# Kernel tuning notes

Measured on AMD Instinct MI355X. Metric: run time of the kernel, lower is better.

The kernel has to match this reference:

```python
import jax, jax.numpy as jnp
import numpy as np

N_TOKENS = 32768
DIM = 4096
N_EXPERTS = 64
TOPK = 2
UPDATE_BIAS_RATE = 0.001
ROUTE_SCALE = 1.0


def setup_inputs() -> dict:
    key = jax.random.key(0)
    k1, k2 = jax.random.split(key)
    x = jax.random.normal(k1, (N_TOKENS, DIM), dtype=jnp.float32)
    # gate projection weight, as in nn.Parameter(torch.empty(E, dim)) + kaiming init
    weight = jax.random.normal(k2, (N_EXPERTS, DIM), dtype=jnp.float32) * 0.02
    bias = jnp.zeros((N_EXPERTS,), dtype=jnp.float32)          # registered buffer
    target_dist = jnp.full((N_EXPERTS,), 1.0 / N_EXPERTS, dtype=jnp.float32)
    return {"x": x, "weight": weight, "bias": bias, "target_dist": target_dist}


def reference(x, weight, bias, target_dist):
    # scores = linear(nan_to_num(x), W) + bias, softmax in fp32
    xc = jnp.nan_to_num(x, nan=0.0)
    scores = (xc @ weight.T + bias).astype(jnp.float32)        # [N, E]
    probs = jax.nn.softmax(scores, axis=-1)                    # [N, E]
    # top-k: gathered values equal the top-k probabilities
    topv, indices = jax.lax.top_k(probs, TOPK)                 # [N, K], [N, K]
    weights = topv / jnp.sum(topv, axis=-1, keepdims=True)
    weights = weights * ROUTE_SCALE
    # load-balancing stats: bincount with float weights == segment_sum
    expert_weights_sum = jax.ops.segment_sum(
        weights.reshape(-1), indices.reshape(-1), num_segments=N_EXPERTS)
    total_weights = expert_weights_sum.sum()
    load_error = target_dist * total_weights - expert_weights_sum
    new_bias = bias + UPDATE_BIAS_RATE * (load_error / total_weights)
    return weights.astype(x.dtype), indices, new_bias
```

## Files before the change

### kernel.cpp

```cpp
#include <hip/hip_runtime.h>
#include <math.h>

#define N_TOKENS 32768
#define DIM      4096
#define NE       64
#define TM       64
#define BK       128
#define KHALF    (DIM / 2)
#define NBLK_MAIN (N_TOKENS / TM * 2)
#define NBLK_POST (N_TOKENS / 256)
#define EPS_GAP  2e-3f
#define REFINE_BLOCKS 1024

#define WOFF     65664
#define WL_OFF   16384
#define PART_OFF 128
#define PSC_OFF  524288
#define WFRAG_ELEMS (512 * 512)

typedef __bf16 bf16x8 __attribute__((ext_vector_type(8)));
typedef float  f32x16 __attribute__((ext_vector_type(16)));

__global__ __launch_bounds__(256) void prep_w(
    const float* __restrict__ w, float* __restrict__ ws)
{
    __bf16* whi = (__bf16*)(ws + WOFF);
    __bf16* wlo = whi + WFRAG_ELEMS;
    const int tid  = blockIdx.x * 256 + threadIdx.x;
    const int f    = tid >> 6, lane = tid & 63;
    const int nt   = f & 1,    K16  = f >> 1;
    const int e    = nt * 32 + (lane & 31);
    const int k    = K16 * 16 + (lane >> 5) * 8;
    const float4 a = *(const float4*)(w + (size_t)e * DIM + k);
    const float4 b = *(const float4*)(w + (size_t)e * DIM + k + 4);
    const float v[8] = {a.x, a.y, a.z, a.w, b.x, b.y, b.z, b.w};
    __bf16 h[8], l[8];
    #pragma unroll
    for (int i = 0; i < 8; ++i) {
        h[i] = (__bf16)v[i];
        l[i] = (__bf16)(v[i] - (float)h[i]);
    }
    *(bf16x8*)(whi + (size_t)tid * 8) = *(bf16x8*)h;
    *(bf16x8*)(wlo + (size_t)tid * 8) = *(bf16x8*)l;
}

__device__ __forceinline__ unsigned pack_pair(float f0, float f1, float& r0, float& r1) {
    const unsigned u0 = __float_as_uint(f0), u1 = __float_as_uint(f1);
    const unsigned h0 = u0 & 0xFFFF0000u,   h1 = u1 & 0xFFFF0000u;
    r0 = f0 - __uint_as_float(h0);
    r1 = f1 - __uint_as_float(h1);
    return (u0 >> 16) | h1;
}
__device__ __forceinline__ void cvt8(const float4 a, const float4 b, uint4& h, uint4& l) {
    float r0, r1, r2, r3, r4, r5, r6, r7;
    h.x = pack_pair(a.x, a.y, r0, r1);
    h.y = pack_pair(a.z, a.w, r2, r3);
    h.z = pack_pair(b.x, b.y, r4, r5);
    h.w = pack_pair(b.z, b.w, r6, r7);
    l.x = (__float_as_uint(r0) >> 16) | (__float_as_uint(r1) & 0xFFFF0000u);
    l.y = (__float_as_uint(r2) >> 16) | (__float_as_uint(r3) & 0xFFFF0000u);
    l.z = (__float_as_uint(r4) >> 16) | (__float_as_uint(r5) & 0xFFFF0000u);
    l.w = (__float_as_uint(r6) >> 16) | (__float_as_uint(r7) & 0xFFFF0000u);
}

__device__ __forceinline__ void gload_lds16(const float* g, float* lds) {
    __builtin_amdgcn_global_load_lds(
        (const __attribute__((address_space(1))) unsigned*)g,
        (__attribute__((address_space(3))) unsigned*)lds, 16, 0, 0);
}

__global__ __launch_bounds__(256) void gate_main(
    const float* __restrict__ x, float* __restrict__ ws)
{
    __shared__ __align__(16) float xs[TM * BK];

    const __bf16* whi = (const __bf16*)(ws + WOFF);
    const __bf16* wlo = whi + WFRAG_ELEMS;
    float*        psc = ws + PSC_OFF;

    const int t    = threadIdx.x;
    const int lane = t & 63;
    const int wave = t >> 6;
    const int mt   = wave >> 1;
    const int nt   = wave & 1;
    const int kh   = blockIdx.x & 1;
    const int tb   = (blockIdx.x >> 1) * TM;
    const int kbeg = kh * KHALF;

    const int l31 = lane & 31, lhi = lane >> 5;

    size_t sbase[8];
    #pragma unroll
    for (int wl = 0; wl < 8; ++wl) {
        const int row = wave * 16 + wl * 2 + lhi;
        const int col = l31 ^ (row & 31);
        sbase[wl] = (size_t)(tb + row) * DIM + kbeg + col * 4;
    }

    const int a_row = mt * 32 + l31;

    f32x16 acc0, acc12;
    #pragma unroll
    for (int i = 0; i < 16; ++i) { acc0[i] = 0.f; acc12[i] = 0.f; }

    for (int s = 0; s < KHALF / BK; ++s) {
        #pragma unroll
        for (int wl = 0; wl < 8; ++wl)
            gload_lds16(x + sbase[wl] + s * BK, &xs[(wave * 16 + wl * 2) * BK]);
        __syncthreads();

        const int K16c = (kbeg + s * BK) >> 4;
        #pragma unroll
        for (int ks = 0; ks < 8; ++ks) {
            const int s0 = ks * 4 + (lhi << 1);
            const float4 fa = *(const float4*)&xs[a_row * BK + ((s0 ^ l31) << 2)];
            const float4 fb = *(const float4*)&xs[a_row * BK + (((s0 + 1) ^ l31) << 2)];
            uint4 h, l;
            cvt8(fa, fb, h, l);
            const size_t bidx = ((size_t)((K16c + ks) * 2 + nt) * 64 + lane) * 8;
            const bf16x8 bh = *(const bf16x8*)(whi + bidx);
            const bf16x8 bl = *(const bf16x8*)(wlo + bidx);
            const bf16x8 ah = __builtin_bit_cast(bf16x8, h);
            const bf16x8 al = __builtin_bit_cast(bf16x8, l);
            acc0  = __builtin_amdgcn_mfma_f32_32x32x16_bf16(ah, bh, acc0,  0, 0, 0);
            acc12 = __builtin_amdgcn_mfma_f32_32x32x16_bf16(al, bh, acc12, 0, 0, 0);
            acc12 = __builtin_amdgcn_mfma_f32_32x32x16_bf16(ah, bl, acc12, 0, 0, 0);
        }
        __syncthreads();
    }

    float* p = psc + (size_t)kh * N_TOKENS * NE + (size_t)tb * NE;
    #pragma unroll
    for (int r = 0; r < 16; ++r) {
        const int tok = mt * 32 + (r & 3) + 8 * (r >> 2) + 4 * lhi;
        p[(size_t)tok * NE + nt * 32 + l31] = acc0[r] + acc12[r];
    }
}

__global__ __launch_bounds__(256) void gate_post(
    const float* __restrict__ bias,
    float* __restrict__ out,
    float* __restrict__ ws)
{
    __shared__ float sbias[NE];
    __shared__ float part[NE];
    unsigned* wl_count = (unsigned*)(ws + 64);
    float*    partials = ws + PART_OFF;
    int*      wl       = (int*)(ws + WL_OFF);
    const float* psc   = ws + PSC_OFF;
    const size_t PL    = (size_t)N_TOKENS * NE;

    const int t = threadIdx.x;
    if (t < NE) { sbias[t] = bias[t]; part[t] = 0.f; }
    __syncthreads();

    const int tok = blockIdx.x * 256 + t;
    const float* p = psc + (size_t)tok * NE;

    float v1 = -3e38f, v2 = -3e38f, v3 = -3e38f;
    int   i1 = 0,      i2 = 0;
    #pragma unroll
    for (int g = 0; g < 16; ++g) {
        const float4 a = *(const float4*)(p + g * 4);
        const float4 b = *(const float4*)(p + PL + g * 4);
        float sv4[4] = {a.x + b.x, a.y + b.y, a.z + b.z, a.w + b.w};
        #pragma unroll
        for (int j = 0; j < 4; ++j) {
            const float sv = sv4[j] + sbias[g * 4 + j];
            const int   e  = g * 4 + j;
            if (sv > v1)      { v3 = v2; v2 = v1; i2 = i1; v1 = sv; i1 = e; }
            else if (sv > v2) { v3 = v2; v2 = sv; i2 = e; }
            else if (sv > v3) { v3 = sv; }
        }
    }
    const bool risky = (v1 - v2 < EPS_GAP) || (v2 - v3 < EPS_GAP);
    if (risky) {
        const int pos = (int)atomicAdd(wl_count, 1u);
        wl[pos] = tok;
    } else {
        const float ex = expf(v2 - v1);
        const float w1 = 1.f / (1.f + ex);
        const float w2 = ex * w1;
        const size_t g = (size_t)tok * 2;
        *(float2*)(out + g)                        = make_float2(w1, w2);
        *(float2*)(out + (size_t)N_TOKENS * 2 + g) = make_float2((float)i1, (float)i2);
        atomicAdd(&part[i1], w1);
        atomicAdd(&part[i2], w2);
    }
    __syncthreads();
    if (t < NE) partials[(size_t)blockIdx.x * NE + t] = part[t];
}

__global__ __launch_bounds__(256) void gate_refine(
    const float* __restrict__ x,
    const float* __restrict__ w,
    const float* __restrict__ bias,
    float* __restrict__ out,
    float* __restrict__ ws)
{
    float*          ews_ref  = ws;
    const unsigned* wl_count = (const unsigned*)(ws + 64);
    const int*      wl       = (const int*)(ws + WL_OFF);

    const int t = threadIdx.x;
    const int e = t >> 2;
    const int q = t & 3;
    __shared__ double sc[NE];

    const unsigned count = *wl_count;
    for (unsigned it = blockIdx.x; it < count; it += gridDim.x) {
        const int tok = wl[it];
        const float* xr = x + (size_t)tok * DIM;
        const float* wr = w + (size_t)e * DIM;
        double s = 0.0;
        const int k0 = q * (DIM / 4), k1 = k0 + DIM / 4;
        for (int k = k0; k < k1; k += 4) {
            const float4 a = *(const float4*)(xr + k);
            const float4 b = *(const float4*)(wr + k);
            s += (double)a.x * (double)b.x;
            s += (double)a.y * (double)b.y;
            s += (double)a.z * (double)b.z;
            s += (double)a.w * (double)b.w;
        }
        s += __shfl_xor(s, 1);
        s += __shfl_xor(s, 2);
        if (q == 0) sc[e] = s + (double)bias[e];
        __syncthreads();

        if (t == 0) {
            double v1 = -1e300, v2 = -1e300;
            int i1 = 0, i2 = 0;
            for (int j = 0; j < NE; ++j) {
                const double sv = sc[j];
                if (sv > v1)      { v2 = v1; i2 = i1; v1 = sv; i1 = j; }
                else if (sv > v2) { v2 = sv; i2 = j; }
            }
            const double ex = exp(v2 - v1);
            const double w1 = 1.0 / (1.0 + ex);
            const double w2 = ex * w1;
            const size_t g = (size_t)tok * 2;
            *(float2*)(out + g)                        = make_float2((float)w1, (float)w2);
            *(float2*)(out + (size_t)N_TOKENS * 2 + g) = make_float2((float)i1, (float)i2);
            atomicAdd(&ews_ref[i1], (float)w1);
            atomicAdd(&ews_ref[i2], (float)w2);
        }
        __syncthreads();
    }
}

__global__ void gate_bias(
    const float* __restrict__ bias,
    const float* __restrict__ target,
    const float* __restrict__ ws,
    float* __restrict__ out)
{
    const int e = threadIdx.x;
    const float* partials = ws + PART_OFF;
    float v = ws[e];
    for (int b = 0; b < NBLK_POST; ++b) v += partials[(size_t)b * NE + e];
    float total = v;
    #pragma unroll
    for (int off = 32; off > 0; off >>= 1)
        total += __shfl_xor(total, off);
    const float nb = bias[e] + 0.001f * ((target[e] * total - v) / total);
    out[(size_t)N_TOKENS * 4 + e] = nb;
}

extern "C" void kernel_launch(void* const* d_in, const int* in_sizes, int n_in,
                              void* d_out, int out_size, void* d_ws, size_t ws_size,
                              hipStream_t stream) {
    const float* x      = (const float*)d_in[0];
    const float* w      = (const float*)d_in[1];
    const float* bias   = (const float*)d_in[2];
    const float* target = (const float*)d_in[3];
    float* out = (float*)d_out;
    float* ws  = (float*)d_ws;

    hipMemsetAsync(ws, 0, 128 * sizeof(float), stream);
    prep_w     <<<128, 256, 0, stream>>>(w, ws);
    gate_main  <<<NBLK_MAIN, 256, 0, stream>>>(x, ws);
    gate_post  <<<NBLK_POST, 256, 0, stream>>>(bias, out, ws);
    gate_refine<<<REFINE_BLOCKS, 256, 0, stream>>>(x, w, bias, out, ws);
    gate_bias  <<<1, 64, 0, stream>>>(bias, target, ws, out);
}
```

Measured before the change: 298.1 us.

## Fuse top-k epilogue into GEMM kernel, drop split-K, double-buffer LDS loads

Removes the split-K partial-score buffer and the separate gate_post kernel. Each block now computes the full K reduction for 64 tokens and runs the top-2 selection and routing weights from scores held in shared memory. The x tiles are streamed with a two-stage LDS double buffer using async global-to-LDS loads, explicit vmcnt waits and barriers, so loads overlap the MFMA work. This cuts global traffic for the scores and one launch, at the cost of half as many blocks and a serialized 64-thread top-k epilogue per block.

Measured after the change: 302.5 us. About the same (+1.5%).

```diff
diff --git a/kernel.cpp b/kernel.cpp
--- a/kernel.cpp
+++ b/kernel.cpp
@@ -5,21 +5,22 @@
 #define DIM      4096
 #define NE       64
 #define TM       64
-#define BK       128
-#define KHALF    (DIM / 2)
-#define NBLK_MAIN (N_TOKENS / TM * 2)
-#define NBLK_POST (N_TOKENS / 256)
+#define BK       64
+#define CHUNKS   (DIM / BK)
+#define NBLK     (N_TOKENS / TM)
 #define EPS_GAP  2e-3f
 #define REFINE_BLOCKS 1024
 
 #define WOFF     65664
-#define WL_OFF   16384
+#define WL_OFF   32896
 #define PART_OFF 128
-#define PSC_OFF  524288
 #define WFRAG_ELEMS (512 * 512)
 
 typedef __bf16 bf16x8 __attribute__((ext_vector_type(8)));
 typedef float  f32x16 __attribute__((ext_vector_type(16)));
+
+#define SCHED0() __builtin_amdgcn_sched_barrier(0)
+#define BAR()    __builtin_amdgcn_s_barrier()
 
 __global__ __launch_bounds__(256) void prep_w(
     const float* __restrict__ w, float* __restrict__ ws)
@@ -70,51 +71,64 @@
 }
 
 __global__ __launch_bounds__(256) void gate_main(
-    const float* __restrict__ x, float* __restrict__ ws)
-{
-    __shared__ __align__(16) float xs[TM * BK];
-
-    const __bf16* whi = (const __bf16*)(ws + WOFF);
-    const __bf16* wlo = whi + WFRAG_ELEMS;
-    float*        psc = ws + PSC_OFF;
+    const float* __restrict__ x, const float* __restrict__ bias,
+    float* __restrict__ out, float* __restrict__ ws)
+{
+    __shared__ __align__(16) float xs[2][TM * BK];
+    __shared__ float sc[TM][68];
+    __shared__ float part[NE];
+    __shared__ float sbias[NE];
+
+    const __bf16* whi  = (const __bf16*)(ws + WOFF);
+    const __bf16* wlo  = whi + WFRAG_ELEMS;
+    unsigned* wl_count = (unsigned*)(ws + 64);
+    float*    partials = ws + PART_OFF;
+    int*      wl       = (int*)(ws + WL_OFF);
 
     const int t    = threadIdx.x;
     const int lane = t & 63;
     const int wave = t >> 6;
     const int mt   = wave >> 1;
     const int nt   = wave & 1;
-    const int kh   = blockIdx.x & 1;
-    const int tb   = (blockIdx.x >> 1) * TM;
-    const int kbeg = kh * KHALF;
-
-    const int l31 = lane & 31, lhi = lane >> 5;
-
-    size_t sbase[8];
-    #pragma unroll
-    for (int wl = 0; wl < 8; ++wl) {
-        const int row = wave * 16 + wl * 2 + lhi;
-        const int col = l31 ^ (row & 31);
-        sbase[wl] = (size_t)(tb + row) * DIM + kbeg + col * 4;
+    const int tb   = blockIdx.x * TM;
+    const int l31  = lane & 31, lhi = lane >> 5;
+
+    if (t < NE) { sbias[t] = bias[t]; part[t] = 0.f; }
+
+    size_t sofs[4];
+    int    dofs[4];
+    #pragma unroll
+    for (int gl = 0; gl < 4; ++gl) {
+        const int row  = wave * 16 + gl * 4 + (lane >> 4);
+        const int slot = (lane & 15) ^ (row & 15);
+        sofs[gl] = (size_t)(tb + row) * DIM + slot * 4;
+        dofs[gl] = (wave * 16 + gl * 4) * BK;
     }
 
     const int a_row = mt * 32 + l31;
+    const int abase = a_row * BK;
+    const int aswz  = a_row & 15;
 
     f32x16 acc0, acc12;
     #pragma unroll
     for (int i = 0; i < 16; ++i) { acc0[i] = 0.f; acc12[i] = 0.f; }
 
-    for (int s = 0; s < KHALF / BK; ++s) {
+    #pragma unroll
+    for (int gl = 0; gl < 4; ++gl) gload_lds16(x + sofs[gl],      &xs[0][dofs[gl]]);
+    #pragma unroll
+    for (int gl = 0; gl < 4; ++gl) gload_lds16(x + sofs[gl] + BK, &xs[1][dofs[gl]]);
+
+    for (int c = 0; c < CHUNKS; ++c) {
+        if (c < CHUNKS - 1) { asm volatile("s_waitcnt vmcnt(4)" ::: "memory"); }
+        else                { asm volatile("s_waitcnt vmcnt(0)" ::: "memory"); }
+        SCHED0(); BAR(); SCHED0();
+
+        const int K16c = c * 4;
         #pragma unroll
-        for (int wl = 0; wl < 8; ++wl)
-            gload_lds16(x + sbase[wl] + s * BK, &xs[(wave * 16 + wl * 2) * BK]);
-        __syncthreads();
-
-        const int K16c = (kbeg + s * BK) >> 4;
-        #pragma unroll
-        for (int ks = 0; ks < 8; ++ks) {
-            const int s0 = ks * 4 + (lhi << 1);
-            const float4 fa = *(const float4*)&xs[a_row * BK + ((s0 ^ l31) << 2)];
-            const float4 fb = *(const float4*)&xs[a_row * BK + (((s0 + 1) ^ l31) << 2)];
+        for (int ks = 0; ks < 4; ++ks) {
+            const int s0 = ks * 4 + lhi * 2;
+            const float4 fa = *(const float4*)&xs[c & 1][abase + ((s0 ^ aswz) << 2)];
+            const float4 fb = *(const float4*)&xs[c & 1][abase + (((s0 + 1) ^ aswz) << 2)];
             uint4 h, l;
             cvt8(fa, fb, h, l);
             const size_t bidx = ((size_t)((K16c + ks) * 2 + nt) * 64 + lane) * 8;
@@ -126,66 +140,49 @@
             acc12 = __builtin_amdgcn_mfma_f32_32x32x16_bf16(al, bh, acc12, 0, 0, 0);
             acc12 = __builtin_amdgcn_mfma_f32_32x32x16_bf16(ah, bl, acc12, 0, 0, 0);
         }
-        __syncthreads();
-    }
-
-    float* p = psc + (size_t)kh * N_TOKENS * NE + (size_t)tb * NE;
+
+        SCHED0(); BAR(); SCHED0();
+        if (c < CHUNKS - 2) {
+            const size_t cofs = (size_t)(c + 2) * BK;
+            #pragma unroll
+            for (int gl = 0; gl < 4; ++gl)
+                gload_lds16(x + sofs[gl] + cofs, &xs[c & 1][dofs[gl]]);
+        }
+    }
+
+    const int e = nt * 32 + l31;
     #pragma unroll
     for (int r = 0; r < 16; ++r) {
         const int tok = mt * 32 + (r & 3) + 8 * (r >> 2) + 4 * lhi;
-        p[(size_t)tok * NE + nt * 32 + l31] = acc0[r] + acc12[r];
-    }
-}
-
-__global__ __launch_bounds__(256) void gate_post(
-    const float* __restrict__ bias,
-    float* __restrict__ out,
-    float* __restrict__ ws)
-{
-    __shared__ float sbias[NE];
-    __shared__ float part[NE];
-    unsigned* wl_count = (unsigned*)(ws + 64);
-    float*    partials = ws + PART_OFF;
-    int*      wl       = (int*)(ws + WL_OFF);
-    const float* psc   = ws + PSC_OFF;
-    const size_t PL    = (size_t)N_TOKENS * NE;
-
-    const int t = threadIdx.x;
-    if (t < NE) { sbias[t] = bias[t]; part[t] = 0.f; }
+        sc[tok][e] = acc0[r] + acc12[r];
+    }
     __syncthreads();
 
-    const int tok = blockIdx.x * 256 + t;
-    const float* p = psc + (size_t)tok * NE;
-
-    float v1 = -3e38f, v2 = -3e38f, v3 = -3e38f;
-    int   i1 = 0,      i2 = 0;
-    #pragma unroll
-    for (int g = 0; g < 16; ++g) {
-        const float4 a = *(const float4*)(p + g * 4);
-        const float4 b = *(const float4*)(p + PL + g * 4);
-        float sv4[4] = {a.x + b.x, a.y + b.y, a.z + b.z, a.w + b.w};
-        #pragma unroll
-        for (int j = 0; j < 4; ++j) {
-            const float sv = sv4[j] + sbias[g * 4 + j];
-            const int   e  = g * 4 + j;
-            if (sv > v1)      { v3 = v2; v2 = v1; i2 = i1; v1 = sv; i1 = e; }
-            else if (sv > v2) { v3 = v2; v2 = sv; i2 = e; }
-            else if (sv > v3) { v3 = sv; }
-        }
-    }
-    const bool risky = (v1 - v2 < EPS_GAP) || (v2 - v3 < EPS_GAP);
-    if (risky) {
-        const int pos = (int)atomicAdd(wl_count, 1u);
-        wl[pos] = tok;
-    } else {
-        const float ex = expf(v2 - v1);
-        const float w1 = 1.f / (1.f + ex);
-        const float w2 = ex * w1;
-        const size_t g = (size_t)tok * 2;
-        *(float2*)(out + g)                        = make_float2(w1, w2);
-        *(float2*)(out + (size_t)N_TOKENS * 2 + g) = make_float2((float)i1, (float)i2);
-        atomicAdd(&part[i1], w1);
-        atomicAdd(&part[i2], w2);
+    if (t < TM) {
+        const int tok = t;
+        float v1 = -3e38f, v2 = -3e38f, v3 = -3e38f;
+        int   i1 = 0,      i2 = 0;
+        #pragma unroll 8
+        for (int ei = 0; ei < NE; ++ei) {
+            const float s = sc[tok][ei] + sbias[ei];
+            if (s > v1)      { v3 = v2; v2 = v1; i2 = i1; v1 = s; i1 = ei; }
+            else if (s > v2) { v3 = v2; v2 = s;  i2 = ei; }
+            else if (s > v3) { v3 = s; }
+        }
+        const bool risky = (v1 - v2 < EPS_GAP) || (v2 - v3 < EPS_GAP);
+        if (risky) {
+            const int pos = (int)atomicAdd(wl_count, 1u);
+            wl[pos] = tb + tok;
+        } else {
+            const float ex = expf(v2 - v1);
+            const float w1 = 1.f / (1.f + ex);
+            const float w2 = ex * w1;
+            const size_t g = (size_t)(tb + tok) * 2;
+            *(float2*)(out + g)                        = make_float2(w1, w2);
+            *(float2*)(out + (size_t)N_TOKENS * 2 + g) = make_float2((float)i1, (float)i2);
+            atomicAdd(&part[i1], w1);
+            atomicAdd(&part[i2], w2);
+        }
     }
     __syncthreads();
     if (t < NE) partials[(size_t)blockIdx.x * NE + t] = part[t];
@@ -257,7 +254,7 @@
     const int e = threadIdx.x;
     const float* partials = ws + PART_OFF;
     float v = ws[e];
-    for (int b = 0; b < NBLK_POST; ++b) v += partials[(size_t)b * NE + e];
+    for (int b = 0; b < NBLK; ++b) v += partials[(size_t)b * NE + e];
     float total = v;
     #pragma unroll
     for (int off = 32; off > 0; off >>= 1)
@@ -278,8 +275,7 @@
 
     hipMemsetAsync(ws, 0, 128 * sizeof(float), stream);
     prep_w     <<<128, 256, 0, stream>>>(w, ws);
-    gate_main  <<<NBLK_MAIN, 256, 0, stream>>>(x, ws);
-    gate_post  <<<NBLK_POST, 256, 0, stream>>>(bias, out, ws);
+    gate_main  <<<NBLK, 256, 0, stream>>>(x, bias, out, ws);
     gate_refine<<<REFINE_BLOCKS, 256, 0, stream>>>(x, w, bias, out, ws);
     gate_bias  <<<1, 64, 0, stream>>>(bias, target, ws, out);
 }
```

## Restructure gate GEMM into 4-way K split with double-buffered async staging

Applied to the files above, without the earlier changes.

Rewrites the main gate GEMM kernel to split K four ways across blocks, with 128-thread blocks where each wave owns 32 tokens and all 64 experts. X tiles are double-buffered through LDS with direct global-to-LDS loads, and W fragments are prefetched into registers, using explicit waitcnt and scheduling barriers so loads overlap MFMA work. The aim is to hide memory latency on the bandwidth-bound x read without block-wide syncs. In exchange, the score partials workspace grows from two to four planes, so the post kernel must read twice as much partial data.

Measured after the change: 296.0 us. Within noise of the previous version (-0.7%).

```diff
diff --git a/kernel.cpp b/kernel.cpp
--- a/kernel.cpp
+++ b/kernel.cpp
@@ -4,10 +4,11 @@
 #define N_TOKENS 32768
 #define DIM      4096
 #define NE       64
-#define TM       64
-#define BK       128
-#define KHALF    (DIM / 2)
-#define NBLK_MAIN (N_TOKENS / TM * 2)
+#define KS       4
+#define KSPAN    (DIM / KS)
+#define BKF      32
+#define NCH      (KSPAN / BKF)
+#define NBLK_MAIN (N_TOKENS / 64 * KS)
 #define NBLK_POST (N_TOKENS / 256)
 #define EPS_GAP  2e-3f
 #define REFINE_BLOCKS 1024
@@ -20,6 +21,8 @@
 
 typedef __bf16 bf16x8 __attribute__((ext_vector_type(8)));
 typedef float  f32x16 __attribute__((ext_vector_type(16)));
+
+#define SB0() __builtin_amdgcn_sched_barrier(0)
 
 __global__ __launch_bounds__(256) void prep_w(
     const float* __restrict__ w, float* __restrict__ ws)
@@ -69,10 +72,12 @@
         (__attribute__((address_space(3))) unsigned*)lds, 16, 0, 0);
 }
 
-__global__ __launch_bounds__(256) void gate_main(
+struct BS { bf16x8 h[2][2]; bf16x8 l[2][2]; };
+
+__global__ __launch_bounds__(128) void gate_main(
     const float* __restrict__ x, float* __restrict__ ws)
 {
-    __shared__ __align__(16) float xs[TM * BK];
+    __shared__ __align__(16) float xsf[4096];
 
     const __bf16* whi = (const __bf16*)(ws + WOFF);
     const __bf16* wlo = whi + WFRAG_ELEMS;
@@ -80,60 +85,96 @@
 
     const int t    = threadIdx.x;
     const int lane = t & 63;
-    const int wave = t >> 6;
-    const int mt   = wave >> 1;
-    const int nt   = wave & 1;
-    const int kh   = blockIdx.x & 1;
-    const int tb   = (blockIdx.x >> 1) * TM;
-    const int kbeg = kh * KHALF;
-
-    const int l31 = lane & 31, lhi = lane >> 5;
-
-    size_t sbase[8];
-    #pragma unroll
-    for (int wl = 0; wl < 8; ++wl) {
-        const int row = wave * 16 + wl * 2 + lhi;
-        const int col = l31 ^ (row & 31);
-        sbase[wl] = (size_t)(tb + row) * DIM + kbeg + col * 4;
-    }
-
-    const int a_row = mt * 32 + l31;
-
-    f32x16 acc0, acc12;
-    #pragma unroll
-    for (int i = 0; i < 16; ++i) { acc0[i] = 0.f; acc12[i] = 0.f; }
-
-    for (int s = 0; s < KHALF / BK; ++s) {
-        #pragma unroll
-        for (int wl = 0; wl < 8; ++wl)
-            gload_lds16(x + sbase[wl] + s * BK, &xs[(wave * 16 + wl * 2) * BK]);
-        __syncthreads();
-
-        const int K16c = (kbeg + s * BK) >> 4;
-        #pragma unroll
-        for (int ks = 0; ks < 8; ++ks) {
-            const int s0 = ks * 4 + (lhi << 1);
-            const float4 fa = *(const float4*)&xs[a_row * BK + ((s0 ^ l31) << 2)];
-            const float4 fb = *(const float4*)&xs[a_row * BK + (((s0 + 1) ^ l31) << 2)];
-            uint4 h, l;
-            cvt8(fa, fb, h, l);
-            const size_t bidx = ((size_t)((K16c + ks) * 2 + nt) * 64 + lane) * 8;
-            const bf16x8 bh = *(const bf16x8*)(whi + bidx);
-            const bf16x8 bl = *(const bf16x8*)(wlo + bidx);
-            const bf16x8 ah = __builtin_bit_cast(bf16x8, h);
-            const bf16x8 al = __builtin_bit_cast(bf16x8, l);
-            acc0  = __builtin_amdgcn_mfma_f32_32x32x16_bf16(ah, bh, acc0,  0, 0, 0);
-            acc12 = __builtin_amdgcn_mfma_f32_32x32x16_bf16(al, bh, acc12, 0, 0, 0);
-            acc12 = __builtin_amdgcn_mfma_f32_32x32x16_bf16(ah, bl, acc12, 0, 0, 0);
-        }
-        __syncthreads();
-    }
-
-    float* p = psc + (size_t)kh * N_TOKENS * NE + (size_t)tb * NE;
+    const int w    = t >> 6;
+    const int tile = blockIdx.x >> 2;
+    const int kq   = blockIdx.x & 3;
+    const int tb   = tile * 64 + w * 32;
+    const int kbeg = kq * KSPAN;
+    const int l31  = lane & 31, lhi = lane >> 5;
+    const int dbase = w * 2048;
+
+    size_t sofs[4];
+    #pragma unroll
+    for (int g = 0; g < 4; ++g) {
+        const int row = g * 8 + (lane >> 3);
+        const int col = ((lane & 7) ^ (lane >> 3)) * 4;
+        sofs[g] = (size_t)(tb + row) * DIM + kbeg + col;
+    }
+
+    const int arow  = l31;
+    const int aswz  = arow & 7;
+
+    f32x16 acc0, acc1;
+    #pragma unroll
+    for (int i = 0; i < 16; ++i) { acc0[i] = 0.f; acc1[i] = 0.f; }
+
+    BS BA, BB;
+
+    #define LOADB(B, c) {                                                     \
+        _Pragma("unroll")                                                     \
+        for (int ks = 0; ks < 2; ++ks) {                                      \
+            _Pragma("unroll")                                                 \
+            for (int nt = 0; nt < 2; ++nt) {                                  \
+                const size_t f = (size_t)((kq * 64 + (c) * 2 + ks) * 2 + nt); \
+                (B).h[ks][nt] = *(const bf16x8*)(whi + (f * 64 + lane) * 8);  \
+                (B).l[ks][nt] = *(const bf16x8*)(wlo + (f * 64 + lane) * 8);  \
+            }                                                                 \
+        } }
+
+    #define STAGE(c, p) {                                                     \
+        _Pragma("unroll")                                                     \
+        for (int g = 0; g < 4; ++g)                                           \
+            gload_lds16(x + sofs[g] + (size_t)(c) * BKF,                      \
+                        &xsf[dbase + (p) * 1024 + g * 256]); }
+
+    #define COMPUTE(p, B) {                                                   \
+        const int ab = dbase + (p) * 1024 + arow * 32;                        \
+        _Pragma("unroll")                                                     \
+        for (int ks = 0; ks < 2; ++ks) {                                      \
+            const int s0 = ks * 4 + lhi * 2;                                  \
+            const float4 fa = *(const float4*)&xsf[ab + ((s0 ^ aswz) << 2)];  \
+            const float4 fb = *(const float4*)&xsf[ab + (((s0+1) ^ aswz) << 2)]; \
+            uint4 hh, ll;                                                     \
+            cvt8(fa, fb, hh, ll);                                             \
+            const bf16x8 ah = __builtin_bit_cast(bf16x8, hh);                 \
+            const bf16x8 al = __builtin_bit_cast(bf16x8, ll);                 \
+            acc0 = __builtin_amdgcn_mfma_f32_32x32x16_bf16(ah, (B).h[ks][0], acc0, 0,0,0); \
+            acc1 = __builtin_amdgcn_mfma_f32_32x32x16_bf16(ah, (B).h[ks][1], acc1, 0,0,0); \
+            acc0 = __builtin_amdgcn_mfma_f32_32x32x16_bf16(al, (B).h[ks][0], acc0, 0,0,0); \
+            acc1 = __builtin_amdgcn_mfma_f32_32x32x16_bf16(al, (B).h[ks][1], acc1, 0,0,0); \
+            acc0 = __builtin_amdgcn_mfma_f32_32x32x16_bf16(ah, (B).l[ks][0], acc0, 0,0,0); \
+            acc1 = __builtin_amdgcn_mfma_f32_32x32x16_bf16(ah, (B).l[ks][1], acc1, 0,0,0); \
+        } }
+
+    LOADB(BA, 0); STAGE(0, 0); LOADB(BB, 1); STAGE(1, 1);
+
+    for (int cc = 0; cc < NCH / 2; ++cc) {
+        const int c0 = 2 * cc;
+        asm volatile("s_waitcnt vmcnt(12)" ::: "memory");
+        SB0();
+        COMPUTE(0, BA);
+        SB0();
+        { const int cn = (c0 + 2 < NCH) ? c0 + 2 : NCH - 1;
+          LOADB(BA, cn); STAGE(cn, 0); }
+        SB0();
+        asm volatile("s_waitcnt vmcnt(12)" ::: "memory");
+        SB0();
+        COMPUTE(1, BB);
+        SB0();
+        { const int cn = (c0 + 3 < NCH) ? c0 + 3 : NCH - 1;
+          LOADB(BB, cn); STAGE(cn, 1); }
+        SB0();
+    }
+    #undef LOADB
+    #undef STAGE
+    #undef COMPUTE
+
+    float* p = psc + ((size_t)kq * N_TOKENS + tb) * NE;
     #pragma unroll
     for (int r = 0; r < 16; ++r) {
-        const int tok = mt * 32 + (r & 3) + 8 * (r >> 2) + 4 * lhi;
-        p[(size_t)tok * NE + nt * 32 + l31] = acc0[r] + acc12[r];
+        const int tok = (r & 3) + 8 * (r >> 2) + 4 * lhi;
+        p[(size_t)tok * NE + l31]      = acc0[r];
+        p[(size_t)tok * NE + l31 + 32] = acc1[r];
     }
 }
 
@@ -163,7 +204,10 @@
     for (int g = 0; g < 16; ++g) {
         const float4 a = *(const float4*)(p + g * 4);
         const float4 b = *(const float4*)(p + PL + g * 4);
-        float sv4[4] = {a.x + b.x, a.y + b.y, a.z + b.z, a.w + b.w};
+        const float4 c = *(const float4*)(p + 2 * PL + g * 4);
+        const float4 d = *(const float4*)(p + 3 * PL + g * 4);
+        float sv4[4] = {(a.x + b.x) + (c.x + d.x), (a.y + b.y) + (c.y + d.y),
+                        (a.z + b.z) + (c.z + d.z), (a.w + b.w) + (c.w + d.w)};
         #pragma unroll
         for (int j = 0; j < 4; ++j) {
             const float sv = sv4[j] + sbias[g * 4 + j];
@@ -278,7 +322,7 @@
 
     hipMemsetAsync(ws, 0, 128 * sizeof(float), stream);
     prep_w     <<<128, 256, 0, stream>>>(w, ws);
-    gate_main  <<<NBLK_MAIN, 256, 0, stream>>>(x, ws);
+    gate_main  <<<NBLK_MAIN, 128, 0, stream>>>(x, ws);
     gate_post  <<<NBLK_POST, 256, 0, stream>>>(bias, out, ws);
     gate_refine<<<REFINE_BLOCKS, 256, 0, stream>>>(x, w, bias, out, ws);
     gate_bias  <<<1, 64, 0, stream>>>(bias, target, ws, out);
```
